# Performance work log

Hardware: AMD Instinct MI355X
Metric: run time of the kernel (lower is better)

## Reference

```python
import jax, jax.numpy as jnp
import numpy as np


def _conv1x1(x, w, b):
    # x: [B,C,H,W], w: [O,C], b: [O] -> [B,O,H,W]
    return jnp.einsum('oc,bchw->bohw', w, x) + b[None, :, None, None]


def setup_inputs() -> dict:
    key = jax.random.key(0)
    ks = jax.random.split(key, 9)
    B, C, O, H, W = 8, 192, 96, 64, 64
    s_in = 1.0 / np.sqrt(C)
    s_out = 1.0 / np.sqrt(O)
    return {
        'x': jax.random.normal(ks[0], (B, C, H, W), dtype=jnp.float32),
        'g_w': jax.random.normal(ks[1], (O, C), dtype=jnp.float32) * s_in,
        'g_b': jax.random.normal(ks[2], (O,), dtype=jnp.float32) * s_in,
        'theta_w': jax.random.normal(ks[3], (O, C), dtype=jnp.float32) * s_in,
        'theta_b': jax.random.normal(ks[4], (O,), dtype=jnp.float32) * s_in,
        'phi_w': jax.random.normal(ks[5], (O, C), dtype=jnp.float32) * s_in,
        'phi_b': jax.random.normal(ks[6], (O,), dtype=jnp.float32) * s_in,
        'W_w': jax.random.normal(ks[7], (C, O), dtype=jnp.float32) * s_out,
        'W_b': jax.random.normal(ks[8], (C,), dtype=jnp.float32) * s_out,
    }


def reference(x, g_w, g_b, theta_w, theta_b, phi_w, phi_b, W_w, W_b):
    B, C, H, W = x.shape
    O = g_w.shape[0]
    N = H * W
    # 1x1 conv projections, flattened to [B, O, N]
    g_x = _conv1x1(x, g_w, g_b).reshape(B, O, N)          # [B,O,N]
    theta_x = _conv1x1(x, theta_w, theta_b).reshape(B, O, N)
    phi_x = _conv1x1(x, phi_w, phi_b).reshape(B, O, N)
    # scores f1[b,n,m] = theta[:, :, n] . phi[:, :, m]
    f1 = jnp.einsum('bon,bom->bnm', theta_x, phi_x)       # [B,N,N]
    f_div_C = jax.nn.softmax(f1, axis=-1)
    # y[b,n,o] = sum_m f[b,n,m] * g[b,o,m]
    y = jnp.einsum('bnm,bom->bon', f_div_C, g_x)          # [B,O,N]
    y = y.reshape(B, O, H, W)
    W_y = _conv1x1(y, W_w, W_b)                           # [B,C,H,W]
    return W_y + x
```

## Files before the change

### kernel.cpp

```cpp
#include <hip/hip_runtime.h>

typedef unsigned short u16;
typedef unsigned int u32;
typedef float f32x4 __attribute__((ext_vector_type(4)));
typedef float f32x16 __attribute__((ext_vector_type(16)));
typedef _Float16 h16x8 __attribute__((ext_vector_type(8)));
typedef u32 u32x4 __attribute__((ext_vector_type(4)));
typedef u32 u32x2 __attribute__((ext_vector_type(2)));
typedef u16 u16x4 __attribute__((ext_vector_type(4)));

#define NB 8
#define CC 192
#define OO 96
#define NN 4096
#define NSPLIT 3
#define XPAD 200
#define LOG2E 1.4426950408889634f

static __device__ __forceinline__ u16 f2h(float f) {
  _Float16 h = (_Float16)f;
  return __builtin_bit_cast(u16, h);
}
static __device__ __forceinline__ void gl_lds16(const u16* g, u16* l) {
  __builtin_amdgcn_global_load_lds(
      (const __attribute__((address_space(1))) void*)g,
      (__attribute__((address_space(3))) void*)l, 16, 0, 0);
}
static __device__ __forceinline__ float exp2_raw(float x) {
  float r;
  asm("v_exp_f32 %0, %1" : "=v"(r) : "v"(x));
  return r;
}
static __device__ __forceinline__ void plane_swap(u32& a, u32& b) {
  u32x2 r = __builtin_amdgcn_permlane32_swap(a, b, false, false);
  a = r[0]; b = r[1];
}
static __device__ __forceinline__ float half_combine_max(float x) {
  u32 a = __builtin_bit_cast(u32, x), b = a;
  plane_swap(a, b);
  return fmaxf(__builtin_bit_cast(float, a), __builtin_bit_cast(float, b));
}
static __device__ __forceinline__ float half_combine_sum(float x) {
  u32 a = __builtin_bit_cast(u32, x), b = a;
  plane_swap(a, b);
  return __builtin_bit_cast(float, a) + __builtin_bit_cast(float, b);
}
static __device__ __forceinline__ float max3f(float a, float b, float c) {
  return fmaxf(fmaxf(a, b), c);
}

__global__ __launch_bounds__(256) void proj_kernel(
    const float* __restrict__ x,
    const float* __restrict__ g_w, const float* __restrict__ g_b,
    const float* __restrict__ th_w, const float* __restrict__ th_b,
    const float* __restrict__ ph_w, const float* __restrict__ ph_b,
    u16* __restrict__ QB, u16* __restrict__ KA, u16* __restrict__ VA)
{
  __shared__ __align__(16) u16 Xs[64][XPAD];
  __shared__ __align__(16) u16 Ws[96][XPAD];
  const int b = blockIdx.y, n0 = blockIdx.x * 64, tid = threadIdx.x;
  const int lane = tid & 63, wv = tid >> 6, l15 = lane & 15, lg = lane >> 4;

  #pragma unroll
  for (int it = 0; it < 12; ++it) {
    int idx = tid + it * 256;
    int c = idx >> 4, q = idx & 15;
    float4 v = *(const float4*)(x + ((size_t)(b * CC + c)) * NN + n0 + q * 4);
    Xs[q * 4 + 0][c] = f2h(v.x); Xs[q * 4 + 1][c] = f2h(v.y);
    Xs[q * 4 + 2][c] = f2h(v.z); Xs[q * 4 + 3][c] = f2h(v.w);
  }

  for (int p = 0; p < 3; ++p) {
    const float* w    = (p == 0) ? th_w : (p == 1) ? ph_w : g_w;
    const float* bias = (p == 0) ? th_b : (p == 1) ? ph_b : g_b;
    const float scale = (p == 0) ? LOG2E : 1.0f;
    __syncthreads();
    #pragma unroll
    for (int it = 0; it < 18; ++it) {
      int idx = tid + it * 256;
      int r = idx / 48, q = idx % 48;
      float4 v = *(const float4*)(w + r * CC + q * 4);
      u16x4 hh; hh[0] = f2h(v.x * scale); hh[1] = f2h(v.y * scale);
      hh[2] = f2h(v.z * scale); hh[3] = f2h(v.w * scale);
      *(u16x4*)&Ws[r][q * 4] = hh;
    }
    __syncthreads();

    f32x4 acc[6];
    #pragma unroll
    for (int of = 0; of < 6; ++of) acc[of] = (f32x4){0.f, 0.f, 0.f, 0.f};
    #pragma unroll
    for (int ks = 0; ks < 6; ++ks) {
      h16x8 xa = *(const h16x8*)&Xs[wv * 16 + l15][ks * 32 + lg * 8];
      #pragma unroll
      for (int of = 0; of < 6; ++of) {
        h16x8 wf = *(const h16x8*)&Ws[of * 16 + l15][ks * 32 + lg * 8];
        if (p < 2) acc[of] = __builtin_amdgcn_mfma_f32_16x16x32_f16(xa, wf, acc[of], 0, 0, 0);
        else       acc[of] = __builtin_amdgcn_mfma_f32_16x16x32_f16(wf, xa, acc[of], 0, 0, 0);
      }
    }

    if (p < 2) {
      u16* dst = (p == 0) ? QB : KA;
      #pragma unroll
      for (int of = 0; of < 6; ++of) {
        int o = of * 16 + l15;
        float bo = bias[o] * scale;
        int kch = of * 2 + (l15 >> 3);
        #pragma unroll
        for (int r = 0; r < 4; ++r) {
          int n = n0 + wv * 16 + lg * 4 + r;
          int idx = (b * 128 + (n >> 5)) * 3072 + (kch * 32 + (n & 31)) * 8 + (o & 7);
          dst[idx] = f2h(acc[of][r] + bo);
        }
      }
    } else {
      #pragma unroll
      for (int of = 0; of < 6; ++of) {
        #pragma unroll
        for (int r = 0; r < 4; ++r) {
          int o = of * 16 + lg * 4 + r;
          int m = n0 + wv * 16 + l15;
          int idx = (b * 256 + (m >> 4)) * 1536 +
                    (((o >> 5) * 2 + ((m >> 3) & 1)) * 32 + (o & 31)) * 8 + (m & 7);
          VA[idx] = f2h(acc[of][r] + bias[o]);
        }
      }
    }
  }
}

static __device__ __forceinline__ void qk_pair(
    const u16* kc, const h16x8* qfA, const h16x8* qfB, int h, int l31,
    f32x16& SA, f32x16& SB)
{
  #pragma unroll
  for (int i = 0; i < 16; ++i) { SA[i] = 0.f; SB[i] = 0.f; }
  #pragma unroll
  for (int ks = 0; ks < 6; ++ks) {
    h16x8 kf = *(const h16x8*)(kc + ((ks * 2 + h) * 32 + l31) * 8);
    SA = __builtin_amdgcn_mfma_f32_32x32x16_f16(kf, qfA[ks], SA, 0, 0, 0);
    SB = __builtin_amdgcn_mfma_f32_32x32x16_f16(kf, qfB[ks], SB, 0, 0, 0);
  }
}

static __device__ __forceinline__ void sm_pair(
    f32x16 SA, f32x16 SB,
    float& mA, float& lA, f32x16* accA,
    float& mB, float& lB, f32x16* accB,
    h16x8* pfA, h16x8* pfB)
{
  float a0 = max3f(SA[0], SA[1], SA[2]),  a1 = max3f(SA[3], SA[4], SA[5]);
  float a2 = max3f(SA[6], SA[7], SA[8]),  a3 = max3f(SA[9], SA[10], SA[11]);
  float a4 = max3f(SA[12], SA[13], SA[14]);
  float pmaxA = half_combine_max(fmaxf(max3f(a0, a1, a2), max3f(a3, a4, SA[15])));
  float b0 = max3f(SB[0], SB[1], SB[2]),  b1 = max3f(SB[3], SB[4], SB[5]);
  float b2 = max3f(SB[6], SB[7], SB[8]),  b3 = max3f(SB[9], SB[10], SB[11]);
  float b4 = max3f(SB[12], SB[13], SB[14]);
  float pmaxB = half_combine_max(fmaxf(max3f(b0, b1, b2), max3f(b3, b4, SB[15])));
  if (__ballot((pmaxA > mA + 11.5416f) || (pmaxB > mB + 11.5416f))) {
    float mnA = fmaxf(mA, pmaxA), scA = exp2_raw(mA - mnA);
    float mnB = fmaxf(mB, pmaxB), scB = exp2_raw(mB - mnB);
    mA = mnA; lA *= scA;
    mB = mnB; lB *= scB;
    #pragma unroll
    for (int ob = 0; ob < 3; ++ob)
      #pragma unroll
      for (int i = 0; i < 16; ++i) { accA[ob][i] *= scA; accB[ob][i] *= scB; }
  }
  #pragma unroll
  for (int i = 0; i < 16; ++i) { SA[i] = exp2_raw(SA[i] - mA); SB[i] = exp2_raw(SB[i] - mB); }
  u32 pkA[8], pkB[8];
  #pragma unroll
  for (int i = 0; i < 8; ++i) {
    pkA[i] = __builtin_bit_cast(u32, __builtin_amdgcn_cvt_pkrtz(SA[2 * i], SA[2 * i + 1]));
    pkB[i] = __builtin_bit_cast(u32, __builtin_amdgcn_cvt_pkrtz(SB[2 * i], SB[2 * i + 1]));
  }
  #pragma unroll
  for (int st = 8; st >= 1; st >>= 1)
    #pragma unroll
    for (int i = 0; i < 8; ++i)
      if (i < st) { SA[i] += SA[i + st]; SB[i] += SB[i + st]; }
  lA += half_combine_sum(SA[0]);
  lB += half_combine_sum(SB[0]);
  plane_swap(pkA[0], pkA[2]); plane_swap(pkA[1], pkA[3]);
  plane_swap(pkA[4], pkA[6]); plane_swap(pkA[5], pkA[7]);
  plane_swap(pkB[0], pkB[2]); plane_swap(pkB[1], pkB[3]);
  plane_swap(pkB[4], pkB[6]); plane_swap(pkB[5], pkB[7]);
  u32x4 a0v = {pkA[0], pkA[1], pkA[2], pkA[3]}, a1v = {pkA[4], pkA[5], pkA[6], pkA[7]};
  u32x4 b0v = {pkB[0], pkB[1], pkB[2], pkB[3]}, b1v = {pkB[4], pkB[5], pkB[6], pkB[7]};
  pfA[0] = __builtin_bit_cast(h16x8, a0v); pfA[1] = __builtin_bit_cast(h16x8, a1v);
  pfB[0] = __builtin_bit_cast(h16x8, b0v); pfB[1] = __builtin_bit_cast(h16x8, b1v);
}

static __device__ __forceinline__ void pv_pair(
    const u16* vc, const h16x8* pfA, const h16x8* pfB, int h, int l31,
    f32x16* accA, f32x16* accB)
{
  #pragma unroll
  for (int s2 = 0; s2 < 2; ++s2) {
    #pragma unroll
    for (int ob = 0; ob < 3; ++ob) {
      h16x8 vf = *(const h16x8*)(vc + (((s2 * 3 + ob) * 2 + h) * 32 + l31) * 8);
      accA[ob] = __builtin_amdgcn_mfma_f32_32x32x16_f16(vf, pfA[s2], accA[ob], 0, 0, 0);
      accB[ob] = __builtin_amdgcn_mfma_f32_32x32x16_f16(vf, pfB[s2], accB[ob], 0, 0, 0);
    }
  }
}

__global__ __launch_bounds__(128, 2) void attn_kernel(
    const u16* __restrict__ QB, const u16* __restrict__ KA,
    const u16* __restrict__ VA, u16* __restrict__ yP, float* __restrict__ ml)
{
  __shared__ __align__(16) u16 Ks[2][6144];
  __shared__ __align__(16) u16 Vs[2][6144];
  const int b   = blockIdx.x;
  const int qt  = blockIdx.y;
  const int sp  = blockIdx.z;
  const int tid = threadIdx.x;
  const int lane = tid & 63;
  const int wv  = tid >> 6;
  const int l31 = lane & 31;
  const int h   = lane >> 5;

  const int t_start = (64 * sp) / NSPLIT;
  const int t_end   = (64 * (sp + 1)) / NSPLIT;

  const int ncA = qt * 4 + wv * 2;
  const int ncB = ncA + 1;
  const u16* qbA = QB + (size_t)(b * 128 + ncA) * 3072;
  const u16* qbB = QB + (size_t)(b * 128 + ncB) * 3072;
  h16x8 qfA[6], qfB[6];
  #pragma unroll
  for (int ks = 0; ks < 6; ++ks) {
    qfA[ks] = *(const h16x8*)(qbA + ((ks * 2 + h) * 32 + l31) * 8);
    qfB[ks] = *(const h16x8*)(qbB + ((ks * 2 + h) * 32 + l31) * 8);
  }

  const u16* KAb = KA + (size_t)b * (128 * 3072);
  const u16* VAb = VA + (size_t)b * (256 * 1536);

  f32x16 accA[3], accB[3];
  #pragma unroll
  for (int ob = 0; ob < 3; ++ob)
    #pragma unroll
    for (int i = 0; i < 16; ++i) { accA[ob][i] = 0.f; accB[ob][i] = 0.f; }
  float mA = -3.0e38f, lA = 0.f;
  float mB = -3.0e38f, lB = 0.f;

  {
    const u16* gk = KAb + (size_t)t_start * 6144;
    const u16* gv = VAb + (size_t)t_start * 6144;
    #pragma unroll
    for (int i = 0; i < 6; ++i) gl_lds16(gk + tid * 8 + i * 1024, &Ks[0][tid * 8 + i * 1024]);
    #pragma unroll
    for (int i = 0; i < 6; ++i) gl_lds16(gv + tid * 8 + i * 1024, &Vs[0][tid * 8 + i * 1024]);
  }

  for (int t = t_start; t < t_end; ++t) {
    const int bf = (t - t_start) & 1;
    asm volatile("s_waitcnt vmcnt(0)" ::: "memory");
    __builtin_amdgcn_s_barrier();
    __builtin_amdgcn_sched_barrier(0);
    if (t + 1 < t_end) {
      const u16* gk = KAb + (size_t)(t + 1) * 6144;
      const u16* gv = VAb + (size_t)(t + 1) * 6144;
      #pragma unroll
      for (int i = 0; i < 6; ++i) gl_lds16(gk + tid * 8 + i * 1024, &Ks[bf ^ 1][tid * 8 + i * 1024]);
      #pragma unroll
      for (int i = 0; i < 6; ++i) gl_lds16(gv + tid * 8 + i * 1024, &Vs[bf ^ 1][tid * 8 + i * 1024]);
    }

    f32x16 SA0, SB0, SA1, SB1;
    h16x8 pfA[2], pfB[2];
    qk_pair(&Ks[bf][0],    qfA, qfB, h, l31, SA0, SB0);
    qk_pair(&Ks[bf][3072], qfA, qfB, h, l31, SA1, SB1);
    sm_pair(SA0, SB0, mA, lA, accA, mB, lB, accB, pfA, pfB);
    pv_pair(&Vs[bf][0], pfA, pfB, h, l31, accA, accB);
    sm_pair(SA1, SB1, mA, lA, accA, mB, lB, accB, pfA, pfB);
    pv_pair(&Vs[bf][3072], pfA, pfB, h, l31, accA, accB);
  }

  #pragma unroll
  for (int qq = 0; qq < 2; ++qq) {
    const f32x16* acc = qq ? accB : accA;
    float mR = qq ? mB : mA, lR = qq ? lB : lA;
    float inv = 1.0f / lR;
    int nglob = (qq ? ncB : ncA) * 32 + l31;
    u16* yp = yP + (((size_t)sp * NB + b) * NN + nglob) * OO;
    #pragma unroll
    for (int ob = 0; ob < 3; ++ob) {
      #pragma unroll
      for (int rq = 0; rq < 4; ++rq) {
        int o0 = ob * 32 + rq * 8 + h * 4;
        u32 w0 = __builtin_bit_cast(u32,
            __builtin_amdgcn_cvt_pkrtz(acc[ob][rq * 4 + 0] * inv, acc[ob][rq * 4 + 1] * inv));
        u32 w1 = __builtin_bit_cast(u32,
            __builtin_amdgcn_cvt_pkrtz(acc[ob][rq * 4 + 2] * inv, acc[ob][rq * 4 + 3] * inv));
        uint2 pr; pr.x = w0; pr.y = w1;
        *(uint2*)&yp[o0] = pr;
      }
    }
    if (h == 0) {
      float2 v2; v2.x = mR; v2.y = lR;
      *(float2*)&ml[(((size_t)sp * NB + b) * NN + nglob) * 2] = v2;
    }
  }
}

#define YPAD 104
__global__ __launch_bounds__(256) void outproj_kernel(
    const float* __restrict__ x, const float* __restrict__ Ww,
    const float* __restrict__ Wb, const u16* __restrict__ yP,
    const float* __restrict__ ml, float* __restrict__ out)
{
  __shared__ __align__(16) u16 Wws[CC][YPAD];
  __shared__ __align__(16) u16 Ys[64][YPAD];
  const int b = blockIdx.y, n0 = blockIdx.x * 64, tid = threadIdx.x;
  const int lane = tid & 63, wv = tid >> 6, l15 = lane & 15, lg = lane >> 4;
  const size_t SB = (size_t)NB * NN;

  #pragma unroll
  for (int it = 0; it < 18; ++it) {
    int idx = tid + it * 256;
    int r = idx / 24, q = idx % 24;
    float4 v = *(const float4*)(Ww + r * OO + q * 4);
    u16x4 hh; hh[0] = f2h(v.x); hh[1] = f2h(v.y); hh[2] = f2h(v.z); hh[3] = f2h(v.w);
    *(u16x4*)&Wws[r][q * 4] = hh;
  }
  #pragma unroll
  for (int it = 0; it < 3; ++it) {
    int idx = tid + it * 256;
    int n = idx / 12, q = idx % 12;
    size_t bn = (size_t)b * NN + n0 + n;
    float mm[NSPLIT], ll[NSPLIT];
    float M = -3.0e38f;
    #pragma unroll
    for (int s = 0; s < NSPLIT; ++s) {
      mm[s] = ml[((size_t)s * SB + bn) * 2];
      ll[s] = ml[((size_t)s * SB + bn) * 2 + 1];
      M = fmaxf(M, mm[s]);
    }
    float wsum = 0.f, w[NSPLIT];
    #pragma unroll
    for (int s = 0; s < NSPLIT; ++s) { w[s] = ll[s] * exp2f(mm[s] - M); wsum += w[s]; }
    float rinv = 1.0f / wsum;
    #pragma unroll
    for (int s = 0; s < NSPLIT; ++s) w[s] *= rinv;
    float accv[8];
    #pragma unroll
    for (int e = 0; e < 8; ++e) accv[e] = 0.f;
    #pragma unroll
    for (int s = 0; s < NSPLIT; ++s) {
      h16x8 ys = *(const h16x8*)(yP + ((size_t)s * SB + bn) * OO + q * 8);
      #pragma unroll
      for (int e = 0; e < 8; ++e) accv[e] += w[s] * (float)ys[e];
    }
    u32x4 packed;
    #pragma unroll
    for (int e = 0; e < 4; ++e)
      packed[e] = __builtin_bit_cast(u32,
          __builtin_amdgcn_cvt_pkrtz(accv[2 * e], accv[2 * e + 1]));
    *(u32x4*)&Ys[n][q * 8] = packed;
  }
  __syncthreads();

  f32x4 acc[12];
  #pragma unroll
  for (int cf = 0; cf < 12; ++cf) acc[cf] = (f32x4){0.f, 0.f, 0.f, 0.f};
  #pragma unroll
  for (int ks = 0; ks < 3; ++ks) {
    h16x8 yb = *(const h16x8*)&Ys[wv * 16 + l15][ks * 32 + lg * 8];
    #pragma unroll
    for (int cf = 0; cf < 12; ++cf) {
      h16x8 wa = *(const h16x8*)&Wws[cf * 16 + l15][ks * 32 + lg * 8];
      acc[cf] = __builtin_amdgcn_mfma_f32_16x16x32_f16(wa, yb, acc[cf], 0, 0, 0);
    }
  }
  #pragma unroll
  for (int cf = 0; cf < 12; ++cf) {
    #pragma unroll
    for (int r = 0; r < 4; ++r) {
      int c = cf * 16 + lg * 4 + r;
      size_t off = ((size_t)(b * CC + c)) * NN + n0 + wv * 16 + l15;
      out[off] = acc[cf][r] + x[off] + Wb[c];
    }
  }
}

extern "C" void kernel_launch(void* const* d_in, const int* in_sizes, int n_in,
                              void* d_out, int out_size, void* d_ws, size_t ws_size,
                              hipStream_t stream) {
  const float* x    = (const float*)d_in[0];
  const float* g_w  = (const float*)d_in[1];
  const float* g_b  = (const float*)d_in[2];
  const float* th_w = (const float*)d_in[3];
  const float* th_b = (const float*)d_in[4];
  const float* ph_w = (const float*)d_in[5];
  const float* ph_b = (const float*)d_in[6];
  const float* W_w  = (const float*)d_in[7];
  const float* W_b  = (const float*)d_in[8];
  float* out = (float*)d_out;

  char* ws = (char*)d_ws;
  const size_t projB = (size_t)NB * NN * OO * sizeof(u16);
  u16* QB   = (u16*)ws;
  u16* KA   = (u16*)(ws + projB);
  u16* VA   = (u16*)(ws + 2 * projB);
  u16* yP   = (u16*)(ws + 3 * projB);
  float* ml = (float*)(ws + (3 + NSPLIT) * projB);

  dim3 gproj(64, NB);
  hipLaunchKernelGGL(proj_kernel, gproj, dim3(256), 0, stream,
                     x, g_w, g_b, th_w, th_b, ph_w, ph_b, QB, KA, VA);
  dim3 gattn(NB, 32, NSPLIT);
  hipLaunchKernelGGL(attn_kernel, gattn, dim3(128), 0, stream, QB, KA, VA, yP, ml);
  dim3 gout(64, NB);
  hipLaunchKernelGGL(outproj_kernel, gout, dim3(256), 0, stream, x, W_w, W_b, yP, ml, out);
}
```

Baseline: 103.8 us.

## Run attention as single-wave blocks with finer K/V chunks and no barriers

The attention kernel moves from 128-thread blocks, where two waves share 64-key K/V tiles, to 64-thread single-wave blocks that each stream 32-key chunks. The grid doubles in the query dimension to match. Because each wave loads its own tiles, the s_barrier disappears and the wait becomes a partial vmcnt, so the current chunk can be consumed while the next one is still in flight. In exchange, K/V tiles are no longer shared between waves, so global/L2 traffic doubles, and each loop iteration does less work per pipeline step.

```diff
diff --git a/kernel.cpp b/kernel.cpp
--- a/kernel.cpp
+++ b/kernel.cpp
@@ -208,25 +208,23 @@
   }
 }
 
-__global__ __launch_bounds__(128, 2) void attn_kernel(
+__global__ __launch_bounds__(64, 2) void attn_kernel(
     const u16* __restrict__ QB, const u16* __restrict__ KA,
     const u16* __restrict__ VA, u16* __restrict__ yP, float* __restrict__ ml)
 {
-  __shared__ __align__(16) u16 Ks[2][6144];
-  __shared__ __align__(16) u16 Vs[2][6144];
+  __shared__ __align__(16) u16 Ks[2][3072];
+  __shared__ __align__(16) u16 Vs[2][3072];
   const int b   = blockIdx.x;
-  const int qt  = blockIdx.y;
+  const int qp  = blockIdx.y;
   const int sp  = blockIdx.z;
   const int tid = threadIdx.x;
-  const int lane = tid & 63;
-  const int wv  = tid >> 6;
-  const int l31 = lane & 31;
-  const int h   = lane >> 5;
-
-  const int t_start = (64 * sp) / NSPLIT;
-  const int t_end   = (64 * (sp + 1)) / NSPLIT;
-
-  const int ncA = qt * 4 + wv * 2;
+  const int l31 = tid & 31;
+  const int h   = tid >> 5;
+
+  const int c_start = (128 * sp) / NSPLIT;
+  const int c_end   = (128 * (sp + 1)) / NSPLIT;
+
+  const int ncA = qp * 2;
   const int ncB = ncA + 1;
   const u16* qbA = QB + (size_t)(b * 128 + ncA) * 3072;
   const u16* qbB = QB + (size_t)(b * 128 + ncB) * 3072;
@@ -249,36 +247,35 @@
   float mB = -3.0e38f, lB = 0.f;
 
   {
-    const u16* gk = KAb + (size_t)t_start * 6144;
-    const u16* gv = VAb + (size_t)t_start * 6144;
-    #pragma unroll
-    for (int i = 0; i < 6; ++i) gl_lds16(gk + tid * 8 + i * 1024, &Ks[0][tid * 8 + i * 1024]);
-    #pragma unroll
-    for (int i = 0; i < 6; ++i) gl_lds16(gv + tid * 8 + i * 1024, &Vs[0][tid * 8 + i * 1024]);
-  }
-
-  for (int t = t_start; t < t_end; ++t) {
-    const int bf = (t - t_start) & 1;
-    asm volatile("s_waitcnt vmcnt(0)" ::: "memory");
-    __builtin_amdgcn_s_barrier();
+    const u16* gk = KAb + (size_t)c_start * 3072;
+    const u16* gv = VAb + (size_t)c_start * 3072;
+    #pragma unroll
+    for (int i = 0; i < 6; ++i) gl_lds16(gk + tid * 8 + i * 512, &Ks[0][tid * 8 + i * 512]);
+    #pragma unroll
+    for (int i = 0; i < 6; ++i) gl_lds16(gv + tid * 8 + i * 512, &Vs[0][tid * 8 + i * 512]);
+  }
+
+  for (int c = c_start; c < c_end; ++c) {
+    const int bf = (c - c_start) & 1;
     __builtin_amdgcn_sched_barrier(0);
-    if (t + 1 < t_end) {
-      const u16* gk = KAb + (size_t)(t + 1) * 6144;
-      const u16* gv = VAb + (size_t)(t + 1) * 6144;
-      #pragma unroll
-      for (int i = 0; i < 6; ++i) gl_lds16(gk + tid * 8 + i * 1024, &Ks[bf ^ 1][tid * 8 + i * 1024]);
-      #pragma unroll
-      for (int i = 0; i < 6; ++i) gl_lds16(gv + tid * 8 + i * 1024, &Vs[bf ^ 1][tid * 8 + i * 1024]);
-    }
-
-    f32x16 SA0, SB0, SA1, SB1;
+    if (c + 1 < c_end) {
+      const u16* gk = KAb + (size_t)(c + 1) * 3072;
+      const u16* gv = VAb + (size_t)(c + 1) * 3072;
+      #pragma unroll
+      for (int i = 0; i < 6; ++i) gl_lds16(gk + tid * 8 + i * 512, &Ks[bf ^ 1][tid * 8 + i * 512]);
+      #pragma unroll
+      for (int i = 0; i < 6; ++i) gl_lds16(gv + tid * 8 + i * 512, &Vs[bf ^ 1][tid * 8 + i * 512]);
+      asm volatile("s_waitcnt vmcnt(12)" ::: "memory");
+    } else {
+      asm volatile("s_waitcnt vmcnt(0)" ::: "memory");
+    }
+    __builtin_amdgcn_sched_barrier(0);
+
+    f32x16 SA, SB;
     h16x8 pfA[2], pfB[2];
-    qk_pair(&Ks[bf][0],    qfA, qfB, h, l31, SA0, SB0);
-    qk_pair(&Ks[bf][3072], qfA, qfB, h, l31, SA1, SB1);
-    sm_pair(SA0, SB0, mA, lA, accA, mB, lB, accB, pfA, pfB);
+    qk_pair(&Ks[bf][0], qfA, qfB, h, l31, SA, SB);
+    sm_pair(SA, SB, mA, lA, accA, mB, lB, accB, pfA, pfB);
     pv_pair(&Vs[bf][0], pfA, pfB, h, l31, accA, accB);
-    sm_pair(SA1, SB1, mA, lA, accA, mB, lB, accB, pfA, pfB);
-    pv_pair(&Vs[bf][3072], pfA, pfB, h, l31, accA, accB);
   }
 
   #pragma unroll
@@ -413,8 +410,8 @@
   dim3 gproj(64, NB);
   hipLaunchKernelGGL(proj_kernel, gproj, dim3(256), 0, stream,
                      x, g_w, g_b, th_w, th_b, ph_w, ph_b, QB, KA, VA);
-  dim3 gattn(NB, 32, NSPLIT);
-  hipLaunchKernelGGL(attn_kernel, gattn, dim3(128), 0, stream, QB, KA, VA, yP, ml);
+  dim3 gattn(NB, 64, NSPLIT);
+  hipLaunchKernelGGL(attn_kernel, gattn, dim3(64), 0, stream, QB, KA, VA, yP, ml);
   dim3 gout(64, NB);
   hipLaunchKernelGGL(outproj_kernel, gout, dim3(256), 0, stream, x, W_w, W_b, yP, ml, out);
 }
```

After: 108.9 us. 1.05x slower.
